# Kernel optimization log

Hardware: AMD Instinct MI355X
Metric: run time of the kernel (lower is better)

Reference implementation:

```python
import jax, jax.numpy as jnp
import numpy as np

B, T, D, H = 8, 1024, 512, 8
HD = D // H  # per-head hidden = embed_dim // n_head = 64
EPS = 1e-5


def setup_inputs() -> dict:
    key = jax.random.key(0)
    ks = jax.random.split(key, 8)
    x = jax.random.normal(ks[0], (B, T, D), dtype=jnp.float32)
    sc = 1.0 / np.sqrt(D)
    Wq = jax.random.normal(ks[1], (D, H * HD), dtype=jnp.float32) * sc
    Wk = jax.random.normal(ks[2], (D, H * HD), dtype=jnp.float32) * sc
    Wp = jax.random.normal(ks[3], (H * HD, D), dtype=jnp.float32) * sc
    bq = jnp.zeros((H * HD,), jnp.float32)
    bk = jnp.zeros((H * HD,), jnp.float32)
    bp = jnp.zeros((D,), jnp.float32)
    w_mlp = jax.random.normal(ks[4], (2 * HD,), dtype=jnp.float32) * 0.1
    ln_g = jnp.ones((D,), jnp.float32)
    ln_b = jnp.zeros((D,), jnp.float32)
    return {"x": x, "Wq": Wq, "bq": bq, "Wk": Wk, "bk": bk,
            "Wp": Wp, "bp": bp, "w_mlp": w_mlp, "ln_g": ln_g, "ln_b": ln_b}


def reference(x, Wq, bq, Wk, bk, Wp, bp, w_mlp, ln_g, ln_b):
    b, t, d = x.shape
    h, hd = H, HD
    # q/k projections, split into heads: [B,T,H,hd]
    qx = (x @ Wq + bq).reshape(b, t, h, hd)
    kx = (x @ Wk + bk).reshape(b, t, h, hd)
    # MLP score: tanh(concat(k_j, q_i) . w) == tanh(k_j.w[:hd] + q_i.w[hd:])
    k_s = jnp.einsum('bkhd,d->bkh', kx, w_mlp[:hd])   # [B,K,H]
    q_s = jnp.einsum('bqhd,d->bqh', qx, w_mlp[hd:])   # [B,Q,H]
    score = jnp.tanh(q_s[:, :, None, :] + k_s[:, None, :, :])  # [B,Q,K,H]
    attn = jax.nn.softmax(score, axis=2)  # softmax over k_len
    # values are the key projection kx (bmm(score, kx) in original)
    out = jnp.einsum('bqkh,bkhd->bqhd', attn, kx).reshape(b, t, h * hd)
    out = out @ Wp + bp  # output projection (dropout is identity at eval)
    # residual + LayerNorm
    y = x + out
    mu = jnp.mean(y, axis=-1, keepdims=True)
    var = jnp.var(y, axis=-1, keepdims=True)
    yn = (y - mu) * jax.lax.rsqrt(var + EPS)
    return yn * ln_g + ln_b
```

## Files before the change

kernel.cpp:

```cpp
#include <hip/hip_runtime.h>
#include <cstddef>

#define TT 1024
#define DDIM 512
#define HH 8
#define NND 128
#define NS 68

typedef __attribute__((ext_vector_type(8))) short bfrag;
typedef __attribute__((ext_vector_type(4))) float facc;

#define SC2   2.8853900817779268f
#define L2E   1.4426950408889634f

static __device__ __forceinline__ unsigned bfrne(float f) {
    unsigned u = __float_as_uint(f);
    return (u + 0x7fffu + ((u >> 16) & 1u)) >> 16;
}
static __device__ __forceinline__ unsigned pack2rne(float a, float b) {
    return bfrne(a) | (bfrne(b) << 16);
}
static __device__ __forceinline__ unsigned pack2hu(float a, float b) {
    return ((__float_as_uint(a) + 0x8000u) >> 16) |
           ((__float_as_uint(b) + 0x8000u) & 0xffff0000u);
}
static __device__ __forceinline__ void gl2lds16(const void* g, void* l) {
    __builtin_amdgcn_global_load_lds(
        (const __attribute__((address_space(1))) unsigned int*)g,
        (__attribute__((address_space(3))) unsigned int*)l, 16, 0, 0);
}
static __device__ __forceinline__ float wt(float t) {
    float r = __builtin_amdgcn_rcpf(t + 1.f);
    return __builtin_amdgcn_exp2f(fmaf(r, -2.f * L2E, L2E));
}

__global__ __launch_bounds__(256) void prepare_kernel(
    const float* __restrict__ x, const float* __restrict__ Wk,
    const float* __restrict__ Wp, const float* __restrict__ Wq,
    const float* __restrict__ bq, const float* __restrict__ wm,
    unsigned short* __restrict__ xb, unsigned short* __restrict__ WkT,
    unsigned short* __restrict__ WpT, unsigned short* __restrict__ vq2b,
    float* __restrict__ qsb2)
{
    const int bx = blockIdx.x, tid = threadIdx.x;
    const int lane = tid & 63, wave = tid >> 6;
    if (bx < 2048) {
        const int row = bx * 4 + wave;
        const float4* xr = (const float4*)(x + (size_t)row * DDIM);
        float4 x0 = xr[lane * 2], x1 = xr[lane * 2 + 1];
        uint4 st;
        st.x = pack2rne(x0.x, x0.y); st.y = pack2rne(x0.z, x0.w);
        st.z = pack2rne(x1.x, x1.y); st.w = pack2rne(x1.z, x1.w);
        int p = lane ^ (row & 7);
        *(uint4*)(xb + (size_t)row * DDIM + p * 8) = st;
    } else if (bx < 2176) {
        int idx = bx - 2048;
        const float* src = (idx & 64) ? Wp : Wk;
        unsigned short* dst = (idx & 64) ? WpT : WkT;
        idx &= 63;
        const int n0 = (idx & 7) * 64, k0 = (idx >> 3) * 64;
        __shared__ float sT[64][65];
        #pragma unroll
        for (int it = 0; it < 4; ++it) {
            int task = it * 256 + tid;
            int kr = task >> 4, c4 = (task & 15) * 4;
            float4 v = *(const float4*)(src + (size_t)(k0 + kr) * DDIM + n0 + c4);
            sT[kr][c4] = v.x; sT[kr][c4 + 1] = v.y; sT[kr][c4 + 2] = v.z; sT[kr][c4 + 3] = v.w;
        }
        __syncthreads();
        #pragma unroll
        for (int it = 0; it < 2; ++it) {
            int task = it * 256 + tid;
            int n = task >> 3, kg = task & 7;
            unsigned u[4];
            #pragma unroll
            for (int jj = 0; jj < 4; ++jj)
                u[jj] = pack2rne(sT[kg * 8 + jj * 2][n], sT[kg * 8 + jj * 2 + 1][n]);
            int p = ((k0 >> 3) + kg) ^ (n & 7);
            uint4 st; st.x = u[0]; st.y = u[1]; st.z = u[2]; st.w = u[3];
            *(uint4*)(dst + (size_t)(n0 + n) * DDIM + p * 8) = st;
        }
    } else {
        int idx = (bx - 2176) * 4 + wave;
        int h = idx >> 9, d = idx & 511;
        float v = Wq[(size_t)d * DDIM + h * 64 + lane] * wm[64 + lane];
        #pragma unroll
        for (int off = 32; off > 0; off >>= 1) v += __shfl_xor(v, off);
        if (lane == 0) vq2b[h * DDIM + d] = (unsigned short)bfrne(v * SC2);
        if (bx == 2176 && tid < HH) {
            float sb = 0.f;
            for (int j = 0; j < 64; ++j)
                sb = fmaf(bq[tid * 64 + j], wm[64 + j], sb);
            qsb2[tid] = sb * SC2;
        }
    }
}

__global__ __launch_bounds__(256) void gemm1_kernel(
    const unsigned short* __restrict__ A, const unsigned short* __restrict__ B,
    const float* __restrict__ bias, unsigned short* __restrict__ kxTg,
    float* __restrict__ ks2, const float* __restrict__ wm,
    const unsigned short* __restrict__ vq2b, const float* __restrict__ qsb2,
    float* __restrict__ qs2)
{
    __shared__ __align__(16) unsigned short smem[50176];
    unsigned short* svq = smem + 49152;
    const int tid = threadIdx.x, lane = tid & 63, wave = tid >> 6;
    const int l15 = lane & 15, quad = lane >> 4;
    const int wr = wave >> 1, wc = wave & 1;
    const int row0 = blockIdx.x * 128, colpair = blockIdx.y;
    const int h = colpair * 2 + wc, n0 = colpair * 128;

    const float qsbh = qsb2[h];
    float bvv[4], wmv[4];
    #pragma unroll
    for (int nt = 0; nt < 4; ++nt) {
        bvv[nt] = bias[h * 64 + nt * 16 + l15];
        wmv[nt] = wm[nt * 16 + l15] * SC2;
    }

    facc acc[4][4]; facc accq[4];
    #pragma unroll
    for (int i = 0; i < 4; ++i) {
        #pragma unroll
        for (int j = 0; j < 4; ++j) { acc[i][j][0]=0.f; acc[i][j][1]=0.f; acc[i][j][2]=0.f; acc[i][j][3]=0.f; }
        accq[i][0]=0.f; accq[i][1]=0.f; accq[i][2]=0.f; accq[i][3]=0.f;
    }

    if (tid < 128)
        gl2lds16(vq2b + colpair * 1024 + tid * 8, &svq[tid * 8]);

    auto stage = [&](int sel, int k0) {
        unsigned short* dA = smem + sel * 16384;
        unsigned short* dB = dA + 8192;
        #pragma unroll
        for (int it = 0; it < 4; ++it) {
            int g = it * 256 + tid;
            int r = g >> 3, kg = g & 7;
            gl2lds16(A + (size_t)(row0 + r) * 512 + k0 + kg * 8, &dA[g * 8]);
            gl2lds16(B + (size_t)(n0 + r) * 512 + k0 + kg * 8, &dB[g * 8]);
        }
    };

    stage(0, 0);
    stage(1, 64);
    #pragma unroll
    for (int kt = 0; kt < 8; ++kt) {
        const int sel = kt % 3;
        if (kt < 6) {
            stage((kt + 2) % 3, (kt + 2) * 64);
            asm volatile("s_waitcnt vmcnt(16)" ::: "memory");
        } else if (kt == 6) {
            asm volatile("s_waitcnt vmcnt(8)" ::: "memory");
        } else {
            asm volatile("s_waitcnt vmcnt(0)" ::: "memory");
        }
        __builtin_amdgcn_s_barrier();
        __builtin_amdgcn_sched_barrier(0);
        const unsigned short* sA = smem + sel * 16384;
        const unsigned short* sB = sA + 8192;
        #pragma unroll
        for (int ks_ = 0; ks_ < 2; ++ks_) {
            int slot = (ks_ * 4 + quad) ^ (l15 & 7);
            bfrag a[4], b[4];
            #pragma unroll
            for (int i = 0; i < 4; ++i) {
                a[i] = *(const bfrag*)&sA[(wr * 64 + i * 16 + l15) * 64 + slot * 8];
                b[i] = *(const bfrag*)&sB[(wc * 64 + i * 16 + l15) * 64 + slot * 8];
            }
            bfrag bvq = *(const bfrag*)&svq[wc * 512 + kt * 64 + ks_ * 32 + quad * 8];
            #pragma unroll
            for (int i = 0; i < 4; ++i) {
                #pragma unroll
                for (int nt = 0; nt < 4; ++nt)
                    acc[i][nt] = __builtin_amdgcn_mfma_f32_16x16x32_bf16(a[i], b[nt], acc[i][nt], 0, 0, 0);
                accq[i] = __builtin_amdgcn_mfma_f32_16x16x32_bf16(a[i], bvq, accq[i], 0, 0, 0);
            }
        }
        __builtin_amdgcn_s_barrier();
        __builtin_amdgcn_sched_barrier(0);
    }
    asm volatile("" ::: "memory");

    const int bb = row0 >> 10, t0 = row0 & 1023;
    float part[4][4];
    #pragma unroll
    for (int i = 0; i < 4; ++i)
        #pragma unroll
        for (int r = 0; r < 4; ++r) part[i][r] = 0.f;

    unsigned short* eT = smem + wc * 8704;
    #pragma unroll
    for (int i = 0; i < 4; ++i) {
        int tr = wr * 64 + i * 16 + quad * 4;
        #pragma unroll
        for (int nt = 0; nt < 4; ++nt) {
            int d = nt * 16 + l15;
            float v0 = acc[i][nt][0] + bvv[nt], v1 = acc[i][nt][1] + bvv[nt];
            float v2 = acc[i][nt][2] + bvv[nt], v3 = acc[i][nt][3] + bvv[nt];
            part[i][0] = fmaf(wmv[nt], v0, part[i][0]);
            part[i][1] = fmaf(wmv[nt], v1, part[i][1]);
            part[i][2] = fmaf(wmv[nt], v2, part[i][2]);
            part[i][3] = fmaf(wmv[nt], v3, part[i][3]);
            *(unsigned*)&eT[d * 136 + tr]     = pack2rne(v0, v1);
            *(unsigned*)&eT[d * 136 + tr + 2] = pack2rne(v2, v3);
        }
    }
    #pragma unroll
    for (int i = 0; i < 4; ++i)
        #pragma unroll
        for (int r = 0; r < 4; ++r) {
            float p = part[i][r];
            p += __shfl_xor(p, 1); p += __shfl_xor(p, 2);
            p += __shfl_xor(p, 4); p += __shfl_xor(p, 8);
            if (l15 == 0) {
                size_t o = (size_t)(bb * HH + h) * TT + t0 + wr * 64 + i * 16 + quad * 4 + r;
                ks2[o] = p;
                qs2[o] = accq[i][r] + qsbh;
            }
        }
    __syncthreads();
    #pragma unroll
    for (int it = 0; it < 8; ++it) {
        int task = it * 256 + tid;
        int hh = task >> 10, rem = task & 1023;
        int col = rem >> 4, seg = rem & 15;
        uint4 v = *(const uint4*)&smem[hh * 8704 + col * 136 + seg * 8];
        int hg = colpair * 2 + hh;
        int g = (t0 >> 3) + seg;
        int p = g ^ (col & 7);
        *(uint4*)(kxTg + ((size_t)(bb * HH + hg) * 64 + col) * TT + p * 8) = v;
    }
}

__global__ __launch_bounds__(256) void nodes_kernel(
    const unsigned short* __restrict__ kxTg, const float* __restrict__ qs2,
    const float* __restrict__ ks2, float* __restrict__ npart)
{
    __shared__ __align__(16) unsigned short kxT[16384];
    __shared__ float tks[256];
    __shared__ float redl[8];
    const int bh = blockIdx.x, kq = blockIdx.y;
    const int tid = threadIdx.x, lane = tid & 63, wave = tid >> 6;
    const int l15 = lane & 15, quad = lane >> 4;
    const unsigned short* kxbase = kxTg + (size_t)bh * 64 * TT;

    #pragma unroll
    for (int it = 0; it < 8; ++it) {
        int g = it * 256 + tid;
        int d = g >> 5, j = g & 31;
        gl2lds16(kxbase + (size_t)d * TT + kq * 256 + j * 8, &kxT[g * 8]);
    }
    float ksv = ks2[(size_t)bh * TT + kq * 256 + tid];
    float4 q4 = ((const float4*)(qs2 + (size_t)bh * TT))[tid];
    tks[tid] = __builtin_amdgcn_exp2f(ksv);
    float mn = fminf(fminf(q4.x, q4.y), fminf(q4.z, q4.w));
    float mx = fmaxf(fmaxf(q4.x, q4.y), fmaxf(q4.z, q4.w));
    #pragma unroll
    for (int off = 32; off > 0; off >>= 1) {
        mn = fminf(mn, __shfl_xor(mn, off));
        mx = fmaxf(mx, __shfl_xor(mx, off));
    }
    if (lane == 0) { redl[wave] = mn; redl[4 + wave] = mx; }
    __syncthreads();
    const float mnv = fminf(fminf(redl[0], redl[1]), fminf(redl[2], redl[3]));
    const float mxv = fmaxf(fmaxf(redl[4], redl[5]), fmaxf(redl[6], redl[7]));
    const float h2v = (mxv - mnv) * (1.f / 127.f);
    const float zA = mnv + (wave * 16 + l15) * h2v;
    const float zB = zA + 64.f * h2v;
    const float tzA = __builtin_amdgcn_exp2f(zA);
    const float tzB = __builtin_amdgcn_exp2f(zB);

    facc acc[2][4]; facc accZ[2];
    #pragma unroll
    for (int g = 0; g < 2; ++g) {
        #pragma unroll
        for (int i = 0; i < 4; ++i) { acc[g][i][0]=0.f; acc[g][i][1]=0.f; acc[g][i][2]=0.f; acc[g][i][3]=0.f; }
        accZ[g][0]=0.f; accZ[g][1]=0.f; accZ[g][2]=0.f; accZ[g][3]=0.f;
    }
    bfrag ones;
    #pragma unroll
    for (int j = 0; j < 8; ++j) ones[j] = (short)0x3F80;

    #pragma unroll
    for (int kst = 0; kst < 8; ++kst) {
        const float* kvp = &tks[kst * 32 + quad * 8];
        float4 kv0 = *(const float4*)kvp;
        float4 kv1 = *(const float4*)(kvp + 4);
        int slot = (kst * 4 + quad) ^ (l15 & 7);
        bfrag bf_[4];
        #pragma unroll
        for (int dt = 0; dt < 4; ++dt)
            bf_[dt] = *(const bfrag*)&kxT[(dt * 16 + l15) * 256 + slot * 8];
        #pragma unroll
        for (int g = 0; g < 2; ++g) {
            float tz = g ? tzB : tzA;
            union { unsigned u[4]; bfrag f; } afu;
            afu.u[0] = pack2hu(wt(tz * kv0.x), wt(tz * kv0.y));
            afu.u[1] = pack2hu(wt(tz * kv0.z), wt(tz * kv0.w));
            afu.u[2] = pack2hu(wt(tz * kv1.x), wt(tz * kv1.y));
            afu.u[3] = pack2hu(wt(tz * kv1.z), wt(tz * kv1.w));
            #pragma unroll
            for (int dt = 0; dt < 4; ++dt)
                acc[g][dt] = __builtin_amdgcn_mfma_f32_16x16x32_bf16(afu.f, bf_[dt], acc[g][dt], 0, 0, 0);
            accZ[g] = __builtin_amdgcn_mfma_f32_16x16x32_bf16(afu.f, ones, accZ[g], 0, 0, 0);
        }
    }
    float* dst = npart + (size_t)(bh * 4 + kq) * (NND * NS);
    #pragma unroll
    for (int g = 0; g < 2; ++g)
        #pragma unroll
        for (int r = 0; r < 4; ++r) {
            int node = g * 64 + wave * 16 + quad * 4 + r;
            #pragma unroll
            for (int dt = 0; dt < 4; ++dt)
                dst[node * NS + dt * 16 + l15] = acc[g][dt][r];
            if (l15 == 0) dst[node * NS + 64] = accZ[g][r];
        }
}

__global__ __launch_bounds__(256) void interp_kernel(
    const float* __restrict__ npart, const float* __restrict__ qs2,
    unsigned short* __restrict__ attb)
{
    __shared__ __align__(16) float nodes[NND * NS];
    __shared__ float redl[8];
    const int bh = blockIdx.x, tq = blockIdx.y;
    const int b = bh >> 3, h = bh & 7;
    const int tid = threadIdx.x, lane = tid & 63, wave = tid >> 6;

    float4 q4 = ((const float4*)(qs2 + (size_t)bh * TT))[tid];
    float mn = fminf(fminf(q4.x, q4.y), fminf(q4.z, q4.w));
    float mx = fmaxf(fmaxf(q4.x, q4.y), fmaxf(q4.z, q4.w));
    #pragma unroll
    for (int off = 32; off > 0; off >>= 1) {
        mn = fminf(mn, __shfl_xor(mn, off));
        mx = fmaxf(mx, __shfl_xor(mx, off));
    }
    if (lane == 0) { redl[wave] = mn; redl[4 + wave] = mx; }
    __syncthreads();
    const float mnv = fminf(fminf(redl[0], redl[1]), fminf(redl[2], redl[3]));
    const float mxv = fmaxf(fmaxf(redl[4], redl[5]), fmaxf(redl[6], redl[7]));
    const float inv127v = 127.f / fmaxf(mxv - mnv, 1e-12f);

    const float4* p0 = (const float4*)(npart + (size_t)(bh * 4 + 0) * (NND * NS));
    const float4* p1 = (const float4*)(npart + (size_t)(bh * 4 + 1) * (NND * NS));
    const float4* p2 = (const float4*)(npart + (size_t)(bh * 4 + 2) * (NND * NS));
    const float4* p3 = (const float4*)(npart + (size_t)(bh * 4 + 3) * (NND * NS));
    #pragma unroll
    for (int it = 0; it < 9; ++it) {
        int g = it * 256 + tid;
        if (g < (NND * NS) / 4) {
            float4 a = p0[g], bb4 = p1[g], c = p2[g], d = p3[g];
            float4 s;
            s.x = a.x + bb4.x + c.x + d.x;
            s.y = a.y + bb4.y + c.y + d.y;
            s.z = a.z + bb4.z + c.z + d.z;
            s.w = a.w + bb4.w + c.w + d.w;
            ((float4*)nodes)[g] = s;
        }
    }
    __syncthreads();

    const float* qsp = qs2 + (size_t)bh * TT;
    #pragma unroll 2
    for (int it = 0; it < 16; ++it) {
        int task = it * 256 + tid;
        int t = tq * 256 + (task >> 4), dp = task & 15;
        float qv = qsp[t];
        float u = (qv - mnv) * inv127v;
        int i = (int)floorf(u) - 1;
        i = i < 0 ? 0 : (i > NND - 4 ? NND - 4 : i);
        float s = u - (float)i;
        float s1 = s - 1.f, s2 = s - 2.f, s3 = s - 3.f;
        float w0 = -s1 * s2 * s3 * (1.f / 6.f);
        float w1 = s * s2 * s3 * 0.5f;
        float w2 = -s * s1 * s3 * 0.5f;
        float w3 = s * s1 * s2 * (1.f / 6.f);
        const float* base = &nodes[i * NS];
        float4 v0 = *(const float4*)(base + 4 * dp);
        float4 v1 = *(const float4*)(base + NS + 4 * dp);
        float4 v2 = *(const float4*)(base + 2 * NS + 4 * dp);
        float4 v3 = *(const float4*)(base + 3 * NS + 4 * dp);
        float zz = w0 * base[64] + w1 * base[NS + 64] + w2 * base[2 * NS + 64] + w3 * base[3 * NS + 64];
        float ox = w0 * v0.x + w1 * v1.x + w2 * v2.x + w3 * v3.x;
        float oy = w0 * v0.y + w1 * v1.y + w2 * v2.y + w3 * v3.y;
        float oz = w0 * v0.z + w1 * v1.z + w2 * v2.z + w3 * v3.z;
        float ow = w0 * v0.w + w1 * v1.w + w2 * v2.w + w3 * v3.w;
        float rz = __builtin_amdgcn_rcpf(zz);
        uint2 st;
        st.x = pack2rne(ox * rz, oy * rz);
        st.y = pack2rne(oz * rz, ow * rz);
        int row = b * TT + t;
        int col = h * 64 + 4 * dp;
        int p = (col >> 3) ^ (row & 7);
        *(uint2*)&attb[(size_t)row * DDIM + p * 8 + (col & 7)] = st;
    }
}

__global__ __launch_bounds__(256) void gemm2_kernel(
    const unsigned short* __restrict__ A, const unsigned short* __restrict__ B,
    const float* __restrict__ bias, unsigned short* __restrict__ yb)
{
    __shared__ __align__(16) unsigned short smem[49152];
    const int tid = threadIdx.x, lane = tid & 63, wave = tid >> 6;
    const int l15 = lane & 15, quad = lane >> 4;
    const int wr = wave >> 1, wc = wave & 1;
    const int row0 = blockIdx.x * 128, col0 = blockIdx.y * 128;

    float bvv[4];
    #pragma unroll
    for (int nt = 0; nt < 4; ++nt) bvv[nt] = bias[col0 + wc * 64 + nt * 16 + l15];

    facc acc[4][4];
    #pragma unroll
    for (int i = 0; i < 4; ++i)
        #pragma unroll
        for (int j = 0; j < 4; ++j) { acc[i][j][0]=0.f; acc[i][j][1]=0.f; acc[i][j][2]=0.f; acc[i][j][3]=0.f; }

    auto stage = [&](int sel, int k0) {
        unsigned short* dA = smem + sel * 16384;
        unsigned short* dB = dA + 8192;
        #pragma unroll
        for (int it = 0; it < 4; ++it) {
            int g = it * 256 + tid;
            int r = g >> 3, kg = g & 7;
            gl2lds16(A + (size_t)(row0 + r) * 512 + k0 + kg * 8, &dA[g * 8]);
            gl2lds16(B + (size_t)(col0 + r) * 512 + k0 + kg * 8, &dB[g * 8]);
        }
    };

    stage(0, 0);
    stage(1, 64);
    #pragma unroll
    for (int kt = 0; kt < 8; ++kt) {
        const int sel = kt % 3;
        if (kt < 6) {
            stage((kt + 2) % 3, (kt + 2) * 64);
            asm volatile("s_waitcnt vmcnt(16)" ::: "memory");
        } else if (kt == 6) {
            asm volatile("s_waitcnt vmcnt(8)" ::: "memory");
        } else {
            asm volatile("s_waitcnt vmcnt(0)" ::: "memory");
        }
        __builtin_amdgcn_s_barrier();
        __builtin_amdgcn_sched_barrier(0);
        const unsigned short* sA = smem + sel * 16384;
        const unsigned short* sB = sA + 8192;
        #pragma unroll
        for (int ks_ = 0; ks_ < 2; ++ks_) {
            int slot = (ks_ * 4 + quad) ^ (l15 & 7);
            bfrag a[4], b[4];
            #pragma unroll
            for (int i = 0; i < 4; ++i) {
                a[i] = *(const bfrag*)&sA[(wr * 64 + i * 16 + l15) * 64 + slot * 8];
                b[i] = *(const bfrag*)&sB[(wc * 64 + i * 16 + l15) * 64 + slot * 8];
            }
            #pragma unroll
            for (int i = 0; i < 4; ++i)
                #pragma unroll
                for (int nt = 0; nt < 4; ++nt)
                    acc[i][nt] = __builtin_amdgcn_mfma_f32_16x16x32_bf16(a[i], b[nt], acc[i][nt], 0, 0, 0);
        }
        __builtin_amdgcn_s_barrier();
        __builtin_amdgcn_sched_barrier(0);
    }
    asm volatile("" ::: "memory");

    unsigned short* yT = smem;
    #pragma unroll
    for (int i = 0; i < 4; ++i) {
        #pragma unroll
        for (int nt = 0; nt < 4; ++nt) {
            int col = wc * 64 + nt * 16 + l15;
            #pragma unroll
            for (int r = 0; r < 4; ++r) {
                int row = wr * 64 + i * 16 + quad * 4 + r;
                yT[row * 136 + col] = (unsigned short)bfrne(acc[i][nt][r] + bvv[nt]);
            }
        }
    }
    __syncthreads();
    #pragma unroll
    for (int it = 0; it < 8; ++it) {
        int task = it * 256 + tid;
        int row = task >> 4, seg = task & 15;
        uint4 v = *(const uint4*)&yT[row * 136 + seg * 8];
        *(uint4*)(yb + (size_t)(row0 + row) * DDIM + col0 + seg * 8) = v;
    }
}

__global__ __launch_bounds__(256) void ln_kernel(
    const unsigned short* __restrict__ yb, const unsigned short* __restrict__ xb,
    const float* __restrict__ g, const float* __restrict__ bet,
    float* __restrict__ out)
{
    const int tid = threadIdx.x, lane = tid & 63, wave = tid >> 6;
    const int row = blockIdx.x * 4 + wave;
    uint4 pv = *(const uint4*)(yb + (size_t)row * DDIM + lane * 8);
    int pgr = lane ^ (row & 7);
    uint4 xv = *(const uint4*)(xb + (size_t)row * DDIM + pgr * 8);
    float y[8];
    const unsigned* pu = (const unsigned*)&pv;
    const unsigned* xu = (const unsigned*)&xv;
    #pragma unroll
    for (int j = 0; j < 4; ++j) {
        y[2*j]   = __uint_as_float(pu[j] << 16)        + __uint_as_float(xu[j] << 16);
        y[2*j+1] = __uint_as_float(pu[j] & 0xffff0000u) + __uint_as_float(xu[j] & 0xffff0000u);
    }
    float s = 0.f, s2 = 0.f;
    #pragma unroll
    for (int i = 0; i < 8; ++i) { s += y[i]; s2 = fmaf(y[i], y[i], s2); }
    #pragma unroll
    for (int off = 32; off > 0; off >>= 1) {
        s += __shfl_xor(s, off);
        s2 += __shfl_xor(s2, off);
    }
    float mu = s * (1.f / 512.f);
    float var = s2 * (1.f / 512.f) - mu * mu;
    float inv = rsqrtf(var + 1e-5f);
    const float4* gp = (const float4*)(g + lane * 8);
    const float4* bp = (const float4*)(bet + lane * 8);
    float4 g0 = gp[0], g1 = gp[1], b0 = bp[0], b1 = bp[1];
    float4 o0, o1;
    o0.x = (y[0] - mu) * inv * g0.x + b0.x; o0.y = (y[1] - mu) * inv * g0.y + b0.y;
    o0.z = (y[2] - mu) * inv * g0.z + b0.z; o0.w = (y[3] - mu) * inv * g0.w + b0.w;
    o1.x = (y[4] - mu) * inv * g1.x + b1.x; o1.y = (y[5] - mu) * inv * g1.y + b1.y;
    o1.z = (y[6] - mu) * inv * g1.z + b1.z; o1.w = (y[7] - mu) * inv * g1.w + b1.w;
    float4* op = (float4*)(out + (size_t)row * DDIM);
    op[lane * 2] = o0; op[lane * 2 + 1] = o1;
}

extern "C" void kernel_launch(void* const* d_in, const int* in_sizes, int n_in,
                              void* d_out, int out_size, void* d_ws, size_t ws_size,
                              hipStream_t stream)
{
    const float* x    = (const float*)d_in[0];
    const float* Wq   = (const float*)d_in[1];
    const float* bq   = (const float*)d_in[2];
    const float* Wk   = (const float*)d_in[3];
    const float* bk   = (const float*)d_in[4];
    const float* Wp   = (const float*)d_in[5];
    const float* bp   = (const float*)d_in[6];
    const float* wm   = (const float*)d_in[7];
    const float* ln_g = (const float*)d_in[8];
    const float* ln_b = (const float*)d_in[9];
    float* out = (float*)d_out;

    float* ws = (float*)d_ws;
    float*          qsb2 = ws;
    unsigned short* vq2b = (unsigned short*)(ws + 64);
    unsigned short* WkT  = (unsigned short*)(ws + 2112);
    unsigned short* WpT  = (unsigned short*)(ws + 133184);
    unsigned short* xb   = (unsigned short*)(ws + 264256);
    unsigned short* kxTg = (unsigned short*)(ws + 2361408);
    float*          qs2  = ws + 4458560;
    float*          ks2  = ws + 4524096;
    unsigned short* attb = (unsigned short*)(ws + 4589632);
    unsigned short* yb   = (unsigned short*)(ws + 6686784);
    float*          npart = ws + 8783936;

    prepare_kernel<<<3200, 256, 0, stream>>>(x, Wk, Wp, Wq, bq, wm,
                                             xb, WkT, WpT, vq2b, qsb2);
    gemm1_kernel<<<dim3(64, 4), 256, 0, stream>>>(xb, WkT, bk, kxTg, ks2, wm,
                                                  vq2b, qsb2, qs2);
    nodes_kernel<<<dim3(64, 4), 256, 0, stream>>>(kxTg, qs2, ks2, npart);
    interp_kernel<<<dim3(64, 4), 256, 0, stream>>>(npart, qs2, attb);
    gemm2_kernel<<<dim3(64, 4), 256, 0, stream>>>(attb, WpT, bp, yb);
    ln_kernel<<<2048, 256, 0, stream>>>(yb, xb, ln_g, ln_b, out);
}
```

Measured before the change: 131.3 us.

## Fuse six stage kernels into one persistent kernel with grid barriers

Result: slower. 290.2 us (+120.9%).

```diff
diff --git a/kernel.cpp b/kernel.cpp
--- a/kernel.cpp
+++ b/kernel.cpp
@@ -6,6 +6,7 @@
 #define HH 8
 #define NND 128
 #define NS 68
+#define NBLK 256
 
 typedef __attribute__((ext_vector_type(8))) short bfrag;
 typedef __attribute__((ext_vector_type(4))) float facc;
@@ -34,520 +35,36 @@
     return __builtin_amdgcn_exp2f(fmaf(r, -2.f * L2E, L2E));
 }
 
-__global__ __launch_bounds__(256) void prepare_kernel(
-    const float* __restrict__ x, const float* __restrict__ Wk,
-    const float* __restrict__ Wp, const float* __restrict__ Wq,
-    const float* __restrict__ bq, const float* __restrict__ wm,
-    unsigned short* __restrict__ xb, unsigned short* __restrict__ WkT,
-    unsigned short* __restrict__ WpT, unsigned short* __restrict__ vq2b,
-    float* __restrict__ qsb2)
+static __device__ __forceinline__ void gsync(unsigned* slot) {
+    __syncthreads();
+    if (threadIdx.x == 0) {
+        __threadfence();
+        __hip_atomic_fetch_add(slot, 1u, __ATOMIC_ACQ_REL, __HIP_MEMORY_SCOPE_AGENT);
+        int guard = 0;
+        while (__hip_atomic_load(slot, __ATOMIC_ACQUIRE, __HIP_MEMORY_SCOPE_AGENT) < NBLK) {
+            __builtin_amdgcn_s_sleep(2);
+            if (++guard > (1 << 20)) break;
+        }
+        __threadfence();
+    }
+    __syncthreads();
+}
+
+struct MArgs {
+    const float* x;  const float* Wq; const float* bq; const float* Wk;
+    const float* bk; const float* Wp; const float* bp; const float* wm;
+    const float* gam; const float* bet; float* out; float* ws; unsigned* bar;
+};
+
+__global__ __launch_bounds__(256) void mega_kernel(MArgs a)
 {
-    const int bx = blockIdx.x, tid = threadIdx.x;
+    __shared__ __align__(16) unsigned char LD[100352];
+
+    const int bid = blockIdx.x, tid = threadIdx.x;
     const int lane = tid & 63, wave = tid >> 6;
-    if (bx < 2048) {
-        const int row = bx * 4 + wave;
-        const float4* xr = (const float4*)(x + (size_t)row * DDIM);
-        float4 x0 = xr[lane * 2], x1 = xr[lane * 2 + 1];
-        uint4 st;
-        st.x = pack2rne(x0.x, x0.y); st.y = pack2rne(x0.z, x0.w);
-        st.z = pack2rne(x1.x, x1.y); st.w = pack2rne(x1.z, x1.w);
-        int p = lane ^ (row & 7);
-        *(uint4*)(xb + (size_t)row * DDIM + p * 8) = st;
-    } else if (bx < 2176) {
-        int idx = bx - 2048;
-        const float* src = (idx & 64) ? Wp : Wk;
-        unsigned short* dst = (idx & 64) ? WpT : WkT;
-        idx &= 63;
-        const int n0 = (idx & 7) * 64, k0 = (idx >> 3) * 64;
-        __shared__ float sT[64][65];
-        #pragma unroll
-        for (int it = 0; it < 4; ++it) {
-            int task = it * 256 + tid;
-            int kr = task >> 4, c4 = (task & 15) * 4;
-            float4 v = *(const float4*)(src + (size_t)(k0 + kr) * DDIM + n0 + c4);
-            sT[kr][c4] = v.x; sT[kr][c4 + 1] = v.y; sT[kr][c4 + 2] = v.z; sT[kr][c4 + 3] = v.w;
-        }
-        __syncthreads();
-        #pragma unroll
-        for (int it = 0; it < 2; ++it) {
-            int task = it * 256 + tid;
-            int n = task >> 3, kg = task & 7;
-            unsigned u[4];
-            #pragma unroll
-            for (int jj = 0; jj < 4; ++jj)
-                u[jj] = pack2rne(sT[kg * 8 + jj * 2][n], sT[kg * 8 + jj * 2 + 1][n]);
-            int p = ((k0 >> 3) + kg) ^ (n & 7);
-            uint4 st; st.x = u[0]; st.y = u[1]; st.z = u[2]; st.w = u[3];
-            *(uint4*)(dst + (size_t)(n0 + n) * DDIM + p * 8) = st;
-        }
-    } else {
-        int idx = (bx - 2176) * 4 + wave;
-        int h = idx >> 9, d = idx & 511;
-        float v = Wq[(size_t)d * DDIM + h * 64 + lane] * wm[64 + lane];
-        #pragma unroll
-        for (int off = 32; off > 0; off >>= 1) v += __shfl_xor(v, off);
-        if (lane == 0) vq2b[h * DDIM + d] = (unsigned short)bfrne(v * SC2);
-        if (bx == 2176 && tid < HH) {
-            float sb = 0.f;
-            for (int j = 0; j < 64; ++j)
-                sb = fmaf(bq[tid * 64 + j], wm[64 + j], sb);
-            qsb2[tid] = sb * SC2;
-        }
-    }
-}
-
-__global__ __launch_bounds__(256) void gemm1_kernel(
-    const unsigned short* __restrict__ A, const unsigned short* __restrict__ B,
-    const float* __restrict__ bias, unsigned short* __restrict__ kxTg,
-    float* __restrict__ ks2, const float* __restrict__ wm,
-    const unsigned short* __restrict__ vq2b, const float* __restrict__ qsb2,
-    float* __restrict__ qs2)
-{
-    __shared__ __align__(16) unsigned short smem[50176];
-    unsigned short* svq = smem + 49152;
-    const int tid = threadIdx.x, lane = tid & 63, wave = tid >> 6;
     const int l15 = lane & 15, quad = lane >> 4;
-    const int wr = wave >> 1, wc = wave & 1;
-    const int row0 = blockIdx.x * 128, colpair = blockIdx.y;
-    const int h = colpair * 2 + wc, n0 = colpair * 128;
-
-    const float qsbh = qsb2[h];
-    float bvv[4], wmv[4];
-    #pragma unroll
-    for (int nt = 0; nt < 4; ++nt) {
-        bvv[nt] = bias[h * 64 + nt * 16 + l15];
-        wmv[nt] = wm[nt * 16 + l15] * SC2;
-    }
-
-    facc acc[4][4]; facc accq[4];
-    #pragma unroll
-    for (int i = 0; i < 4; ++i) {
-        #pragma unroll
-        for (int j = 0; j < 4; ++j) { acc[i][j][0]=0.f; acc[i][j][1]=0.f; acc[i][j][2]=0.f; acc[i][j][3]=0.f; }
-        accq[i][0]=0.f; accq[i][1]=0.f; accq[i][2]=0.f; accq[i][3]=0.f;
-    }
-
-    if (tid < 128)
-        gl2lds16(vq2b + colpair * 1024 + tid * 8, &svq[tid * 8]);
-
-    auto stage = [&](int sel, int k0) {
-        unsigned short* dA = smem + sel * 16384;
-        unsigned short* dB = dA + 8192;
-        #pragma unroll
-        for (int it = 0; it < 4; ++it) {
-            int g = it * 256 + tid;
-            int r = g >> 3, kg = g & 7;
-            gl2lds16(A + (size_t)(row0 + r) * 512 + k0 + kg * 8, &dA[g * 8]);
-            gl2lds16(B + (size_t)(n0 + r) * 512 + k0 + kg * 8, &dB[g * 8]);
-        }
-    };
-
-    stage(0, 0);
-    stage(1, 64);
-    #pragma unroll
-    for (int kt = 0; kt < 8; ++kt) {
-        const int sel = kt % 3;
-        if (kt < 6) {
-            stage((kt + 2) % 3, (kt + 2) * 64);
-            asm volatile("s_waitcnt vmcnt(16)" ::: "memory");
-        } else if (kt == 6) {
-            asm volatile("s_waitcnt vmcnt(8)" ::: "memory");
-        } else {
-            asm volatile("s_waitcnt vmcnt(0)" ::: "memory");
-        }
-        __builtin_amdgcn_s_barrier();
-        __builtin_amdgcn_sched_barrier(0);
-        const unsigned short* sA = smem + sel * 16384;
-        const unsigned short* sB = sA + 8192;
-        #pragma unroll
-        for (int ks_ = 0; ks_ < 2; ++ks_) {
-            int slot = (ks_ * 4 + quad) ^ (l15 & 7);
-            bfrag a[4], b[4];
-            #pragma unroll
-            for (int i = 0; i < 4; ++i) {
-                a[i] = *(const bfrag*)&sA[(wr * 64 + i * 16 + l15) * 64 + slot * 8];
-                b[i] = *(const bfrag*)&sB[(wc * 64 + i * 16 + l15) * 64 + slot * 8];
-            }
-            bfrag bvq = *(const bfrag*)&svq[wc * 512 + kt * 64 + ks_ * 32 + quad * 8];
-            #pragma unroll
-            for (int i = 0; i < 4; ++i) {
-                #pragma unroll
-                for (int nt = 0; nt < 4; ++nt)
-                    acc[i][nt] = __builtin_amdgcn_mfma_f32_16x16x32_bf16(a[i], b[nt], acc[i][nt], 0, 0, 0);
-                accq[i] = __builtin_amdgcn_mfma_f32_16x16x32_bf16(a[i], bvq, accq[i], 0, 0, 0);
-            }
-        }
-        __builtin_amdgcn_s_barrier();
-        __builtin_amdgcn_sched_barrier(0);
-    }
-    asm volatile("" ::: "memory");
-
-    const int bb = row0 >> 10, t0 = row0 & 1023;
-    float part[4][4];
-    #pragma unroll
-    for (int i = 0; i < 4; ++i)
-        #pragma unroll
-        for (int r = 0; r < 4; ++r) part[i][r] = 0.f;
-
-    unsigned short* eT = smem + wc * 8704;
-    #pragma unroll
-    for (int i = 0; i < 4; ++i) {
-        int tr = wr * 64 + i * 16 + quad * 4;
-        #pragma unroll
-        for (int nt = 0; nt < 4; ++nt) {
-            int d = nt * 16 + l15;
-            float v0 = acc[i][nt][0] + bvv[nt], v1 = acc[i][nt][1] + bvv[nt];
-            float v2 = acc[i][nt][2] + bvv[nt], v3 = acc[i][nt][3] + bvv[nt];
-            part[i][0] = fmaf(wmv[nt], v0, part[i][0]);
-            part[i][1] = fmaf(wmv[nt], v1, part[i][1]);
-            part[i][2] = fmaf(wmv[nt], v2, part[i][2]);
-            part[i][3] = fmaf(wmv[nt], v3, part[i][3]);
-            *(unsigned*)&eT[d * 136 + tr]     = pack2rne(v0, v1);
-            *(unsigned*)&eT[d * 136 + tr + 2] = pack2rne(v2, v3);
-        }
-    }
-    #pragma unroll
-    for (int i = 0; i < 4; ++i)
-        #pragma unroll
-        for (int r = 0; r < 4; ++r) {
-            float p = part[i][r];
-            p += __shfl_xor(p, 1); p += __shfl_xor(p, 2);
-            p += __shfl_xor(p, 4); p += __shfl_xor(p, 8);
-            if (l15 == 0) {
-                size_t o = (size_t)(bb * HH + h) * TT + t0 + wr * 64 + i * 16 + quad * 4 + r;
-                ks2[o] = p;
-                qs2[o] = accq[i][r] + qsbh;
-            }
-        }
-    __syncthreads();
-    #pragma unroll
-    for (int it = 0; it < 8; ++it) {
-        int task = it * 256 + tid;
-        int hh = task >> 10, rem = task & 1023;
-        int col = rem >> 4, seg = rem & 15;
-        uint4 v = *(const uint4*)&smem[hh * 8704 + col * 136 + seg * 8];
-        int hg = colpair * 2 + hh;
-        int g = (t0 >> 3) + seg;
-        int p = g ^ (col & 7);
-        *(uint4*)(kxTg + ((size_t)(bb * HH + hg) * 64 + col) * TT + p * 8) = v;
-    }
-}
-
-__global__ __launch_bounds__(256) void nodes_kernel(
-    const unsigned short* __restrict__ kxTg, const float* __restrict__ qs2,
-    const float* __restrict__ ks2, float* __restrict__ npart)
-{
-    __shared__ __align__(16) unsigned short kxT[16384];
-    __shared__ float tks[256];
-    __shared__ float redl[8];
-    const int bh = blockIdx.x, kq = blockIdx.y;
-    const int tid = threadIdx.x, lane = tid & 63, wave = tid >> 6;
-    const int l15 = lane & 15, quad = lane >> 4;
-    const unsigned short* kxbase = kxTg + (size_t)bh * 64 * TT;
-
-    #pragma unroll
-    for (int it = 0; it < 8; ++it) {
-        int g = it * 256 + tid;
-        int d = g >> 5, j = g & 31;
-        gl2lds16(kxbase + (size_t)d * TT + kq * 256 + j * 8, &kxT[g * 8]);
-    }
-    float ksv = ks2[(size_t)bh * TT + kq * 256 + tid];
-    float4 q4 = ((const float4*)(qs2 + (size_t)bh * TT))[tid];
-    tks[tid] = __builtin_amdgcn_exp2f(ksv);
-    float mn = fminf(fminf(q4.x, q4.y), fminf(q4.z, q4.w));
-    float mx = fmaxf(fmaxf(q4.x, q4.y), fmaxf(q4.z, q4.w));
-    #pragma unroll
-    for (int off = 32; off > 0; off >>= 1) {
-        mn = fminf(mn, __shfl_xor(mn, off));
-        mx = fmaxf(mx, __shfl_xor(mx, off));
-    }
-    if (lane == 0) { redl[wave] = mn; redl[4 + wave] = mx; }
-    __syncthreads();
-    const float mnv = fminf(fminf(redl[0], redl[1]), fminf(redl[2], redl[3]));
-    const float mxv = fmaxf(fmaxf(redl[4], redl[5]), fmaxf(redl[6], redl[7]));
-    const float h2v = (mxv - mnv) * (1.f / 127.f);
-    const float zA = mnv + (wave * 16 + l15) * h2v;
-    const float zB = zA + 64.f * h2v;
-    const float tzA = __builtin_amdgcn_exp2f(zA);
-    const float tzB = __builtin_amdgcn_exp2f(zB);
-
-    facc acc[2][4]; facc accZ[2];
-    #pragma unroll
-    for (int g = 0; g < 2; ++g) {
-        #pragma unroll
-        for (int i = 0; i < 4; ++i) { acc[g][i][0]=0.f; acc[g][i][1]=0.f; acc[g][i][2]=0.f; acc[g][i][3]=0.f; }
-        accZ[g][0]=0.f; accZ[g][1]=0.f; accZ[g][2]=0.f; accZ[g][3]=0.f;
-    }
-    bfrag ones;
-    #pragma unroll
-    for (int j = 0; j < 8; ++j) ones[j] = (short)0x3F80;
-
-    #pragma unroll
-    for (int kst = 0; kst < 8; ++kst) {
-        const float* kvp = &tks[kst * 32 + quad * 8];
-        float4 kv0 = *(const float4*)kvp;
-        float4 kv1 = *(const float4*)(kvp + 4);
-        int slot = (kst * 4 + quad) ^ (l15 & 7);
-        bfrag bf_[4];
-        #pragma unroll
-        for (int dt = 0; dt < 4; ++dt)
-            bf_[dt] = *(const bfrag*)&kxT[(dt * 16 + l15) * 256 + slot * 8];
-        #pragma unroll
-        for (int g = 0; g < 2; ++g) {
-            float tz = g ? tzB : tzA;
-            union { unsigned u[4]; bfrag f; } afu;
-            afu.u[0] = pack2hu(wt(tz * kv0.x), wt(tz * kv0.y));
-            afu.u[1] = pack2hu(wt(tz * kv0.z), wt(tz * kv0.w));
-            afu.u[2] = pack2hu(wt(tz * kv1.x), wt(tz * kv1.y));
-            afu.u[3] = pack2hu(wt(tz * kv1.z), wt(tz * kv1.w));
-            #pragma unroll
-            for (int dt = 0; dt < 4; ++dt)
-                acc[g][dt] = __builtin_amdgcn_mfma_f32_16x16x32_bf16(afu.f, bf_[dt], acc[g][dt], 0, 0, 0);
-            accZ[g] = __builtin_amdgcn_mfma_f32_16x16x32_bf16(afu.f, ones, accZ[g], 0, 0, 0);
-        }
-    }
-    float* dst = npart + (size_t)(bh * 4 + kq) * (NND * NS);
-    #pragma unroll
-    for (int g = 0; g < 2; ++g)
-        #pragma unroll
-        for (int r = 0; r < 4; ++r) {
-            int node = g * 64 + wave * 16 + quad * 4 + r;
-            #pragma unroll
-            for (int dt = 0; dt < 4; ++dt)
-                dst[node * NS + dt * 16 + l15] = acc[g][dt][r];
-            if (l15 == 0) dst[node * NS + 64] = accZ[g][r];
-        }
-}
-
-__global__ __launch_bounds__(256) void interp_kernel(
-    const float* __restrict__ npart, const float* __restrict__ qs2,
-    unsigned short* __restrict__ attb)
-{
-    __shared__ __align__(16) float nodes[NND * NS];
-    __shared__ float redl[8];
-    const int bh = blockIdx.x, tq = blockIdx.y;
-    const int b = bh >> 3, h = bh & 7;
-    const int tid = threadIdx.x, lane = tid & 63, wave = tid >> 6;
-
-    float4 q4 = ((const float4*)(qs2 + (size_t)bh * TT))[tid];
-    float mn = fminf(fminf(q4.x, q4.y), fminf(q4.z, q4.w));
-    float mx = fmaxf(fmaxf(q4.x, q4.y), fmaxf(q4.z, q4.w));
-    #pragma unroll
-    for (int off = 32; off > 0; off >>= 1) {
-        mn = fminf(mn, __shfl_xor(mn, off));
-        mx = fmaxf(mx, __shfl_xor(mx, off));
-    }
-    if (lane == 0) { redl[wave] = mn; redl[4 + wave] = mx; }
-    __syncthreads();
-    const float mnv = fminf(fminf(redl[0], redl[1]), fminf(redl[2], redl[3]));
-    const float mxv = fmaxf(fmaxf(redl[4], redl[5]), fmaxf(redl[6], redl[7]));
-    const float inv127v = 127.f / fmaxf(mxv - mnv, 1e-12f);
-
-    const float4* p0 = (const float4*)(npart + (size_t)(bh * 4 + 0) * (NND * NS));
-    const float4* p1 = (const float4*)(npart + (size_t)(bh * 4 + 1) * (NND * NS));
-    const float4* p2 = (const float4*)(npart + (size_t)(bh * 4 + 2) * (NND * NS));
-    const float4* p3 = (const float4*)(npart + (size_t)(bh * 4 + 3) * (NND * NS));
-    #pragma unroll
-    for (int it = 0; it < 9; ++it) {
-        int g = it * 256 + tid;
-        if (g < (NND * NS) / 4) {
-            float4 a = p0[g], bb4 = p1[g], c = p2[g], d = p3[g];
-            float4 s;
-            s.x = a.x + bb4.x + c.x + d.x;
-            s.y = a.y + bb4.y + c.y + d.y;
-            s.z = a.z + bb4.z + c.z + d.z;
-            s.w = a.w + bb4.w + c.w + d.w;
-            ((float4*)nodes)[g] = s;
-        }
-    }
-    __syncthreads();
-
-    const float* qsp = qs2 + (size_t)bh * TT;
-    #pragma unroll 2
-    for (int it = 0; it < 16; ++it) {
-        int task = it * 256 + tid;
-        int t = tq * 256 + (task >> 4), dp = task & 15;
-        float qv = qsp[t];
-        float u = (qv - mnv) * inv127v;
-        int i = (int)floorf(u) - 1;
-        i = i < 0 ? 0 : (i > NND - 4 ? NND - 4 : i);
-        float s = u - (float)i;
-        float s1 = s - 1.f, s2 = s - 2.f, s3 = s - 3.f;
-        float w0 = -s1 * s2 * s3 * (1.f / 6.f);
-        float w1 = s * s2 * s3 * 0.5f;
-        float w2 = -s * s1 * s3 * 0.5f;
-        float w3 = s * s1 * s2 * (1.f / 6.f);
-        const float* base = &nodes[i * NS];
-        float4 v0 = *(const float4*)(base + 4 * dp);
-        float4 v1 = *(const float4*)(base + NS + 4 * dp);
-        float4 v2 = *(const float4*)(base + 2 * NS + 4 * dp);
-        float4 v3 = *(const float4*)(base + 3 * NS + 4 * dp);
-        float zz = w0 * base[64] + w1 * base[NS + 64] + w2 * base[2 * NS + 64] + w3 * base[3 * NS + 64];
-        float ox = w0 * v0.x + w1 * v1.x + w2 * v2.x + w3 * v3.x;
-        float oy = w0 * v0.y + w1 * v1.y + w2 * v2.y + w3 * v3.y;
-        float oz = w0 * v0.z + w1 * v1.z + w2 * v2.z + w3 * v3.z;
-        float ow = w0 * v0.w + w1 * v1.w + w2 * v2.w + w3 * v3.w;
-        float rz = __builtin_amdgcn_rcpf(zz);
-        uint2 st;
-        st.x = pack2rne(ox * rz, oy * rz);
-        st.y = pack2rne(oz * rz, ow * rz);
-        int row = b * TT + t;
-        int col = h * 64 + 4 * dp;
-        int p = (col >> 3) ^ (row & 7);
-        *(uint2*)&attb[(size_t)row * DDIM + p * 8 + (col & 7)] = st;
-    }
-}
-
-__global__ __launch_bounds__(256) void gemm2_kernel(
-    const unsigned short* __restrict__ A, const unsigned short* __restrict__ B,
-    const float* __restrict__ bias, unsigned short* __restrict__ yb)
-{
-    __shared__ __align__(16) unsigned short smem[49152];
-    const int tid = threadIdx.x, lane = tid & 63, wave = tid >> 6;
-    const int l15 = lane & 15, quad = lane >> 4;
-    const int wr = wave >> 1, wc = wave & 1;
-    const int row0 = blockIdx.x * 128, col0 = blockIdx.y * 128;
-
-    float bvv[4];
-    #pragma unroll
-    for (int nt = 0; nt < 4; ++nt) bvv[nt] = bias[col0 + wc * 64 + nt * 16 + l15];
-
-    facc acc[4][4];
-    #pragma unroll
-    for (int i = 0; i < 4; ++i)
-        #pragma unroll
-        for (int j = 0; j < 4; ++j) { acc[i][j][0]=0.f; acc[i][j][1]=0.f; acc[i][j][2]=0.f; acc[i][j][3]=0.f; }
-
-    auto stage = [&](int sel, int k0) {
-        unsigned short* dA = smem + sel * 16384;
-        unsigned short* dB = dA + 8192;
-        #pragma unroll
-        for (int it = 0; it < 4; ++it) {
-            int g = it * 256 + tid;
-            int r = g >> 3, kg = g & 7;
-            gl2lds16(A + (size_t)(row0 + r) * 512 + k0 + kg * 8, &dA[g * 8]);
-            gl2lds16(B + (size_t)(col0 + r) * 512 + k0 + kg * 8, &dB[g * 8]);
-        }
-    };
-
-    stage(0, 0);
-    stage(1, 64);
-    #pragma unroll
-    for (int kt = 0; kt < 8; ++kt) {
-        const int sel = kt % 3;
-        if (kt < 6) {
-            stage((kt + 2) % 3, (kt + 2) * 64);
-            asm volatile("s_waitcnt vmcnt(16)" ::: "memory");
-        } else if (kt == 6) {
-            asm volatile("s_waitcnt vmcnt(8)" ::: "memory");
-        } else {
-            asm volatile("s_waitcnt vmcnt(0)" ::: "memory");
-        }
-        __builtin_amdgcn_s_barrier();
-        __builtin_amdgcn_sched_barrier(0);
-        const unsigned short* sA = smem + sel * 16384;
-        const unsigned short* sB = sA + 8192;
-        #pragma unroll
-        for (int ks_ = 0; ks_ < 2; ++ks_) {
-            int slot = (ks_ * 4 + quad) ^ (l15 & 7);
-            bfrag a[4], b[4];
-            #pragma unroll
-            for (int i = 0; i < 4; ++i) {
-                a[i] = *(const bfrag*)&sA[(wr * 64 + i * 16 + l15) * 64 + slot * 8];
-                b[i] = *(const bfrag*)&sB[(wc * 64 + i * 16 + l15) * 64 + slot * 8];
-            }
-            #pragma unroll
-            for (int i = 0; i < 4; ++i)
-                #pragma unroll
-                for (int nt = 0; nt < 4; ++nt)
-                    acc[i][nt] = __builtin_amdgcn_mfma_f32_16x16x32_bf16(a[i], b[nt], acc[i][nt], 0, 0, 0);
-        }
-        __builtin_amdgcn_s_barrier();
-        __builtin_amdgcn_sched_barrier(0);
-    }
-    asm volatile("" ::: "memory");
-
-    unsigned short* yT = smem;
-    #pragma unroll
-    for (int i = 0; i < 4; ++i) {
-        #pragma unroll
-        for (int nt = 0; nt < 4; ++nt) {
-            int col = wc * 64 + nt * 16 + l15;
-            #pragma unroll
-            for (int r = 0; r < 4; ++r) {
-                int row = wr * 64 + i * 16 + quad * 4 + r;
-                yT[row * 136 + col] = (unsigned short)bfrne(acc[i][nt][r] + bvv[nt]);
-            }
-        }
-    }
-    __syncthreads();
-    #pragma unroll
-    for (int it = 0; it < 8; ++it) {
-        int task = it * 256 + tid;
-        int row = task >> 4, seg = task & 15;
-        uint4 v = *(const uint4*)&yT[row * 136 + seg * 8];
-        *(uint4*)(yb + (size_t)(row0 + row) * DDIM + col0 + seg * 8) = v;
-    }
-}
-
-__global__ __launch_bounds__(256) void ln_kernel(
-    const unsigned short* __restrict__ yb, const unsigned short* __restrict__ xb,
-    const float* __restrict__ g, const float* __restrict__ bet,
-    float* __restrict__ out)
-{
-    const int tid = threadIdx.x, lane = tid & 63, wave = tid >> 6;
-    const int row = blockIdx.x * 4 + wave;
-    uint4 pv = *(const uint4*)(yb + (size_t)row * DDIM + lane * 8);
-    int pgr = lane ^ (row & 7);
-    uint4 xv = *(const uint4*)(xb + (size_t)row * DDIM + pgr * 8);
-    float y[8];
-    const unsigned* pu = (const unsigned*)&pv;
-    const unsigned* xu = (const unsigned*)&xv;
-    #pragma unroll
-    for (int j = 0; j < 4; ++j) {
-        y[2*j]   = __uint_as_float(pu[j] << 16)        + __uint_as_float(xu[j] << 16);
-        y[2*j+1] = __uint_as_float(pu[j] & 0xffff0000u) + __uint_as_float(xu[j] & 0xffff0000u);
-    }
-    float s = 0.f, s2 = 0.f;
-    #pragma unroll
-    for (int i = 0; i < 8; ++i) { s += y[i]; s2 = fmaf(y[i], y[i], s2); }
-    #pragma unroll
-    for (int off = 32; off > 0; off >>= 1) {
-        s += __shfl_xor(s, off);
-        s2 += __shfl_xor(s2, off);
-    }
-    float mu = s * (1.f / 512.f);
-    float var = s2 * (1.f / 512.f) - mu * mu;
-    float inv = rsqrtf(var + 1e-5f);
-    const float4* gp = (const float4*)(g + lane * 8);
-    const float4* bp = (const float4*)(bet + lane * 8);
-    float4 g0 = gp[0], g1 = gp[1], b0 = bp[0], b1 = bp[1];
-    float4 o0, o1;
-    o0.x = (y[0] - mu) * inv * g0.x + b0.x; o0.y = (y[1] - mu) * inv * g0.y + b0.y;
-    o0.z = (y[2] - mu) * inv * g0.z + b0.z; o0.w = (y[3] - mu) * inv * g0.w + b0.w;
-    o1.x = (y[4] - mu) * inv * g1.x + b1.x; o1.y = (y[5] - mu) * inv * g1.y + b1.y;
-    o1.z = (y[6] - mu) * inv * g1.z + b1.z; o1.w = (y[7] - mu) * inv * g1.w + b1.w;
-    float4* op = (float4*)(out + (size_t)row * DDIM);
-    op[lane * 2] = o0; op[lane * 2 + 1] = o1;
-}
-
-extern "C" void kernel_launch(void* const* d_in, const int* in_sizes, int n_in,
-                              void* d_out, int out_size, void* d_ws, size_t ws_size,
-                              hipStream_t stream)
-{
-    const float* x    = (const float*)d_in[0];
-    const float* Wq   = (const float*)d_in[1];
-    const float* bq   = (const float*)d_in[2];
-    const float* Wk   = (const float*)d_in[3];
-    const float* bk   = (const float*)d_in[4];
-    const float* Wp   = (const float*)d_in[5];
-    const float* bp   = (const float*)d_in[6];
-    const float* wm   = (const float*)d_in[7];
-    const float* ln_g = (const float*)d_in[8];
-    const float* ln_b = (const float*)d_in[9];
-    float* out = (float*)d_out;
-
-    float* ws = (float*)d_ws;
+
+    float* ws = a.ws;
     float*          qsb2 = ws;
     unsigned short* vq2b = (unsigned short*)(ws + 64);
     unsigned short* WkT  = (unsigned short*)(ws + 2112);
@@ -560,12 +77,501 @@
     unsigned short* yb   = (unsigned short*)(ws + 6686784);
     float*          npart = ws + 8783936;
 
-    prepare_kernel<<<3200, 256, 0, stream>>>(x, Wk, Wp, Wq, bq, wm,
-                                             xb, WkT, WpT, vq2b, qsb2);
-    gemm1_kernel<<<dim3(64, 4), 256, 0, stream>>>(xb, WkT, bk, kxTg, ks2, wm,
-                                                  vq2b, qsb2, qs2);
-    nodes_kernel<<<dim3(64, 4), 256, 0, stream>>>(kxTg, qs2, ks2, npart);
-    interp_kernel<<<dim3(64, 4), 256, 0, stream>>>(npart, qs2, attb);
-    gemm2_kernel<<<dim3(64, 4), 256, 0, stream>>>(attb, WpT, bp, yb);
-    ln_kernel<<<2048, 256, 0, stream>>>(yb, xb, ln_g, ln_b, out);
-}
+    {
+        #pragma unroll
+        for (int i = 0; i < 8; ++i) {
+            int row = bid * 32 + i * 4 + wave;
+            const float4* xr = (const float4*)(a.x + (size_t)row * DDIM);
+            float4 x0 = xr[lane * 2], x1 = xr[lane * 2 + 1];
+            uint4 st;
+            st.x = pack2rne(x0.x, x0.y); st.y = pack2rne(x0.z, x0.w);
+            st.z = pack2rne(x1.x, x1.y); st.w = pack2rne(x1.z, x1.w);
+            int p = lane ^ (row & 7);
+            *(uint4*)(xb + (size_t)row * DDIM + p * 8) = st;
+        }
+        #pragma unroll
+        for (int e = 0; e < 4; ++e) {
+            int idx = (bid * 4 + wave) * 4 + e;
+            int h = idx >> 9, d = idx & 511;
+            float v = a.Wq[(size_t)d * DDIM + h * 64 + lane] * a.wm[64 + lane];
+            #pragma unroll
+            for (int off = 32; off > 0; off >>= 1) v += __shfl_xor(v, off);
+            if (lane == 0) vq2b[h * DDIM + d] = (unsigned short)bfrne(v * SC2);
+        }
+        if (bid == 0 && tid < HH) {
+            float sb = 0.f;
+            for (int j = 0; j < 64; ++j)
+                sb = fmaf(a.bq[tid * 64 + j], a.wm[64 + j], sb);
+            qsb2[tid] = sb * SC2;
+        }
+        if (bid < 128) {
+            const float* src = (bid & 64) ? a.Wp : a.Wk;
+            unsigned short* dst = (bid & 64) ? WpT : WkT;
+            int idx = bid & 63;
+            const int n0 = (idx & 7) * 64, k0 = (idx >> 3) * 64;
+            float (*sT)[65] = (float(*)[65])LD;
+            #pragma unroll
+            for (int it = 0; it < 4; ++it) {
+                int task = it * 256 + tid;
+                int kr = task >> 4, c4 = (task & 15) * 4;
+                float4 v = *(const float4*)(src + (size_t)(k0 + kr) * DDIM + n0 + c4);
+                sT[kr][c4] = v.x; sT[kr][c4 + 1] = v.y; sT[kr][c4 + 2] = v.z; sT[kr][c4 + 3] = v.w;
+            }
+            __syncthreads();
+            #pragma unroll
+            for (int it = 0; it < 2; ++it) {
+                int task = it * 256 + tid;
+                int n = task >> 3, kg = task & 7;
+                unsigned u[4];
+                #pragma unroll
+                for (int jj = 0; jj < 4; ++jj)
+                    u[jj] = pack2rne(sT[kg * 8 + jj * 2][n], sT[kg * 8 + jj * 2 + 1][n]);
+                int p = ((k0 >> 3) + kg) ^ (n & 7);
+                uint4 st; st.x = u[0]; st.y = u[1]; st.z = u[2]; st.w = u[3];
+                *(uint4*)(dst + (size_t)(n0 + n) * DDIM + p * 8) = st;
+            }
+        }
+    }
+    gsync(a.bar + 0);
+
+    {
+        unsigned short* smem = (unsigned short*)LD;
+        unsigned short* svq  = smem + 49152;
+        const int rt = bid & 63, colpair = bid >> 6;
+        const int wr = wave >> 1, wc = wave & 1;
+        const int row0 = rt * 128;
+        const int h = colpair * 2 + wc, n0 = colpair * 128;
+
+        const float qsbh = qsb2[h];
+        float bvv[4], wmv[4];
+        #pragma unroll
+        for (int nt = 0; nt < 4; ++nt) {
+            bvv[nt] = a.bk[h * 64 + nt * 16 + l15];
+            wmv[nt] = a.wm[nt * 16 + l15] * SC2;
+        }
+
+        facc acc[4][4]; facc accq[4];
+        #pragma unroll
+        for (int i = 0; i < 4; ++i) {
+            #pragma unroll
+            for (int j = 0; j < 4; ++j) { acc[i][j][0]=0.f; acc[i][j][1]=0.f; acc[i][j][2]=0.f; acc[i][j][3]=0.f; }
+            accq[i][0]=0.f; accq[i][1]=0.f; accq[i][2]=0.f; accq[i][3]=0.f;
+        }
+
+        if (tid < 128)
+            gl2lds16(vq2b + colpair * 1024 + tid * 8, &svq[tid * 8]);
+
+        auto stage = [&](int sel, int k0) {
+            unsigned short* dA = smem + sel * 16384;
+            unsigned short* dB = dA + 8192;
+            #pragma unroll
+            for (int it = 0; it < 4; ++it) {
+                int g = it * 256 + tid;
+                int r = g >> 3, kg = g & 7;
+                gl2lds16(xb + (size_t)(row0 + r) * 512 + k0 + kg * 8, &dA[g * 8]);
+                gl2lds16(WkT + (size_t)(n0 + r) * 512 + k0 + kg * 8, &dB[g * 8]);
+            }
+        };
+
+        stage(0, 0);
+        stage(1, 64);
+        #pragma unroll
+        for (int kt = 0; kt < 8; ++kt) {
+            const int sel = kt % 3;
+            if (kt < 6) {
+                stage((kt + 2) % 3, (kt + 2) * 64);
+                asm volatile("s_waitcnt vmcnt(16)" ::: "memory");
+            } else if (kt == 6) {
+                asm volatile("s_waitcnt vmcnt(8)" ::: "memory");
+            } else {
+                asm volatile("s_waitcnt vmcnt(0)" ::: "memory");
+            }
+            __builtin_amdgcn_s_barrier();
+            __builtin_amdgcn_sched_barrier(0);
+            const unsigned short* sA = smem + sel * 16384;
+            const unsigned short* sB = sA + 8192;
+            #pragma unroll
+            for (int ks_ = 0; ks_ < 2; ++ks_) {
+                int slot = (ks_ * 4 + quad) ^ (l15 & 7);
+                bfrag av[4], bv[4];
+                #pragma unroll
+                for (int i = 0; i < 4; ++i) {
+                    av[i] = *(const bfrag*)&sA[(wr * 64 + i * 16 + l15) * 64 + slot * 8];
+                    bv[i] = *(const bfrag*)&sB[(wc * 64 + i * 16 + l15) * 64 + slot * 8];
+                }
+                bfrag bvq = *(const bfrag*)&svq[wc * 512 + kt * 64 + ks_ * 32 + quad * 8];
+                #pragma unroll
+                for (int i = 0; i < 4; ++i) {
+                    #pragma unroll
+                    for (int nt = 0; nt < 4; ++nt)
+                        acc[i][nt] = __builtin_amdgcn_mfma_f32_16x16x32_bf16(av[i], bv[nt], acc[i][nt], 0, 0, 0);
+                    accq[i] = __builtin_amdgcn_mfma_f32_16x16x32_bf16(av[i], bvq, accq[i], 0, 0, 0);
+                }
+            }
+            __builtin_amdgcn_s_barrier();
+            __builtin_amdgcn_sched_barrier(0);
+        }
+        asm volatile("" ::: "memory");
+
+        const int bb = row0 >> 10, t0 = row0 & 1023;
+        float part[4][4];
+        #pragma unroll
+        for (int i = 0; i < 4; ++i)
+            #pragma unroll
+            for (int r = 0; r < 4; ++r) part[i][r] = 0.f;
+
+        unsigned short* eT = smem + wc * 8704;
+        #pragma unroll
+        for (int i = 0; i < 4; ++i) {
+            int tr = wr * 64 + i * 16 + quad * 4;
+            #pragma unroll
+            for (int nt = 0; nt < 4; ++nt) {
+                int d = nt * 16 + l15;
+                float v0 = acc[i][nt][0] + bvv[nt], v1 = acc[i][nt][1] + bvv[nt];
+                float v2 = acc[i][nt][2] + bvv[nt], v3 = acc[i][nt][3] + bvv[nt];
+                part[i][0] = fmaf(wmv[nt], v0, part[i][0]);
+                part[i][1] = fmaf(wmv[nt], v1, part[i][1]);
+                part[i][2] = fmaf(wmv[nt], v2, part[i][2]);
+                part[i][3] = fmaf(wmv[nt], v3, part[i][3]);
+                *(unsigned*)&eT[d * 136 + tr]     = pack2rne(v0, v1);
+                *(unsigned*)&eT[d * 136 + tr + 2] = pack2rne(v2, v3);
+            }
+        }
+        #pragma unroll
+        for (int i = 0; i < 4; ++i)
+            #pragma unroll
+            for (int r = 0; r < 4; ++r) {
+                float p = part[i][r];
+                p += __shfl_xor(p, 1); p += __shfl_xor(p, 2);
+                p += __shfl_xor(p, 4); p += __shfl_xor(p, 8);
+                if (l15 == 0) {
+                    size_t o = (size_t)(bb * HH + h) * TT + t0 + wr * 64 + i * 16 + quad * 4 + r;
+                    ks2[o] = p;
+                    qs2[o] = accq[i][r] + qsbh;
+                }
+            }
+        __syncthreads();
+        #pragma unroll
+        for (int it = 0; it < 8; ++it) {
+            int task = it * 256 + tid;
+            int hh = task >> 10, rem = task & 1023;
+            int col = rem >> 4, seg = rem & 15;
+            uint4 v = *(const uint4*)&smem[hh * 8704 + col * 136 + seg * 8];
+            int hg = colpair * 2 + hh;
+            int g = (t0 >> 3) + seg;
+            int p = g ^ (col & 7);
+            *(uint4*)(kxTg + ((size_t)(bb * HH + hg) * 64 + col) * TT + p * 8) = v;
+        }
+    }
+    gsync(a.bar + 1);
+
+    {
+        unsigned short* kxT = (unsigned short*)LD;
+        float* tks  = (float*)(LD + 32768);
+        float* redl = (float*)(LD + 33792);
+        const int bh = bid & 63, kq = bid >> 6;
+        const unsigned short* kxbase = kxTg + (size_t)bh * 64 * TT;
+
+        #pragma unroll
+        for (int it = 0; it < 8; ++it) {
+            int g = it * 256 + tid;
+            int d = g >> 5, j = g & 31;
+            gl2lds16(kxbase + (size_t)d * TT + kq * 256 + j * 8, &kxT[g * 8]);
+        }
+        float ksv = ks2[(size_t)bh * TT + kq * 256 + tid];
+        float4 q4 = ((const float4*)(qs2 + (size_t)bh * TT))[tid];
+        tks[tid] = __builtin_amdgcn_exp2f(ksv);
+        float mn = fminf(fminf(q4.x, q4.y), fminf(q4.z, q4.w));
+        float mx = fmaxf(fmaxf(q4.x, q4.y), fmaxf(q4.z, q4.w));
+        #pragma unroll
+        for (int off = 32; off > 0; off >>= 1) {
+            mn = fminf(mn, __shfl_xor(mn, off));
+            mx = fmaxf(mx, __shfl_xor(mx, off));
+        }
+        if (lane == 0) { redl[wave] = mn; redl[4 + wave] = mx; }
+        __syncthreads();
+        const float mnv = fminf(fminf(redl[0], redl[1]), fminf(redl[2], redl[3]));
+        const float mxv = fmaxf(fmaxf(redl[4], redl[5]), fmaxf(redl[6], redl[7]));
+        const float h2v = (mxv - mnv) * (1.f / 127.f);
+        const float zA = mnv + (wave * 16 + l15) * h2v;
+        const float zB = zA + 64.f * h2v;
+        const float tzA = __builtin_amdgcn_exp2f(zA);
+        const float tzB = __builtin_amdgcn_exp2f(zB);
+
+        facc acc[2][4]; facc accZ[2];
+        #pragma unroll
+        for (int g = 0; g < 2; ++g) {
+            #pragma unroll
+            for (int i = 0; i < 4; ++i) { acc[g][i][0]=0.f; acc[g][i][1]=0.f; acc[g][i][2]=0.f; acc[g][i][3]=0.f; }
+            accZ[g][0]=0.f; accZ[g][1]=0.f; accZ[g][2]=0.f; accZ[g][3]=0.f;
+        }
+        bfrag ones;
+        #pragma unroll
+        for (int j = 0; j < 8; ++j) ones[j] = (short)0x3F80;
+
+        #pragma unroll
+        for (int kst = 0; kst < 8; ++kst) {
+            const float* kvp = &tks[kst * 32 + quad * 8];
+            float4 kv0 = *(const float4*)kvp;
+            float4 kv1 = *(const float4*)(kvp + 4);
+            int slot = (kst * 4 + quad) ^ (l15 & 7);
+            bfrag bf_[4];
+            #pragma unroll
+            for (int dt = 0; dt < 4; ++dt)
+                bf_[dt] = *(const bfrag*)&kxT[(dt * 16 + l15) * 256 + slot * 8];
+            #pragma unroll
+            for (int g = 0; g < 2; ++g) {
+                float tz = g ? tzB : tzA;
+                union { unsigned u[4]; bfrag f; } afu;
+                afu.u[0] = pack2hu(wt(tz * kv0.x), wt(tz * kv0.y));
+                afu.u[1] = pack2hu(wt(tz * kv0.z), wt(tz * kv0.w));
+                afu.u[2] = pack2hu(wt(tz * kv1.x), wt(tz * kv1.y));
+                afu.u[3] = pack2hu(wt(tz * kv1.z), wt(tz * kv1.w));
+                #pragma unroll
+                for (int dt = 0; dt < 4; ++dt)
+                    acc[g][dt] = __builtin_amdgcn_mfma_f32_16x16x32_bf16(afu.f, bf_[dt], acc[g][dt], 0, 0, 0);
+                accZ[g] = __builtin_amdgcn_mfma_f32_16x16x32_bf16(afu.f, ones, accZ[g], 0, 0, 0);
+            }
+        }
+        float* dst = npart + (size_t)(bh * 4 + kq) * (NND * NS);
+        #pragma unroll
+        for (int g = 0; g < 2; ++g)
+            #pragma unroll
+            for (int r = 0; r < 4; ++r) {
+                int node = g * 64 + wave * 16 + quad * 4 + r;
+                #pragma unroll
+                for (int dt = 0; dt < 4; ++dt)
+                    dst[node * NS + dt * 16 + l15] = acc[g][dt][r];
+                if (l15 == 0) dst[node * NS + 64] = accZ[g][r];
+            }
+    }
+    gsync(a.bar + 2);
+
+    {
+        float* nodesArr = (float*)LD;
+        float* redl = (float*)(LD + 34816);
+        const int bh = bid & 63, tq = bid >> 6;
+        const int b = bh >> 3, h = bh & 7;
+
+        float4 q4 = ((const float4*)(qs2 + (size_t)bh * TT))[tid];
+        float mn = fminf(fminf(q4.x, q4.y), fminf(q4.z, q4.w));
+        float mx = fmaxf(fmaxf(q4.x, q4.y), fmaxf(q4.z, q4.w));
+        #pragma unroll
+        for (int off = 32; off > 0; off >>= 1) {
+            mn = fminf(mn, __shfl_xor(mn, off));
+            mx = fmaxf(mx, __shfl_xor(mx, off));
+        }
+        if (lane == 0) { redl[wave] = mn; redl[4 + wave] = mx; }
+        __syncthreads();
+        const float mnv = fminf(fminf(redl[0], redl[1]), fminf(redl[2], redl[3]));
+        const float mxv = fmaxf(fmaxf(redl[4], redl[5]), fmaxf(redl[6], redl[7]));
+        const float inv127v = 127.f / fmaxf(mxv - mnv, 1e-12f);
+
+        const float4* p0 = (const float4*)(npart + (size_t)(bh * 4 + 0) * (NND * NS));
+        const float4* p1 = (const float4*)(npart + (size_t)(bh * 4 + 1) * (NND * NS));
+        const float4* p2 = (const float4*)(npart + (size_t)(bh * 4 + 2) * (NND * NS));
+        const float4* p3 = (const float4*)(npart + (size_t)(bh * 4 + 3) * (NND * NS));
+        #pragma unroll
+        for (int it = 0; it < 9; ++it) {
+            int g = it * 256 + tid;
+            if (g < (NND * NS) / 4) {
+                float4 av = p0[g], bv = p1[g], cv = p2[g], dv = p3[g];
+                float4 s;
+                s.x = av.x + bv.x + cv.x + dv.x;
+                s.y = av.y + bv.y + cv.y + dv.y;
+                s.z = av.z + bv.z + cv.z + dv.z;
+                s.w = av.w + bv.w + cv.w + dv.w;
+                ((float4*)nodesArr)[g] = s;
+            }
+        }
+        __syncthreads();
+
+        const float* qsp = qs2 + (size_t)bh * TT;
+        #pragma unroll 2
+        for (int it = 0; it < 16; ++it) {
+            int task = it * 256 + tid;
+            int t = tq * 256 + (task >> 4), dp = task & 15;
+            float qv = qsp[t];
+            float u = (qv - mnv) * inv127v;
+            int i = (int)floorf(u) - 1;
+            i = i < 0 ? 0 : (i > NND - 4 ? NND - 4 : i);
+            float s = u - (float)i;
+            float s1 = s - 1.f, s2 = s - 2.f, s3 = s - 3.f;
+            float w0 = -s1 * s2 * s3 * (1.f / 6.f);
+            float w1 = s * s2 * s3 * 0.5f;
+            float w2 = -s * s1 * s3 * 0.5f;
+            float w3 = s * s1 * s2 * (1.f / 6.f);
+            const float* base = &nodesArr[i * NS];
+            float4 v0 = *(const float4*)(base + 4 * dp);
+            float4 v1 = *(const float4*)(base + NS + 4 * dp);
+            float4 v2 = *(const float4*)(base + 2 * NS + 4 * dp);
+            float4 v3 = *(const float4*)(base + 3 * NS + 4 * dp);
+            float zz = w0 * base[64] + w1 * base[NS + 64] + w2 * base[2 * NS + 64] + w3 * base[3 * NS + 64];
+            float ox = w0 * v0.x + w1 * v1.x + w2 * v2.x + w3 * v3.x;
+            float oy = w0 * v0.y + w1 * v1.y + w2 * v2.y + w3 * v3.y;
+            float oz = w0 * v0.z + w1 * v1.z + w2 * v2.z + w3 * v3.z;
+            float ow = w0 * v0.w + w1 * v1.w + w2 * v2.w + w3 * v3.w;
+            float rz = __builtin_amdgcn_rcpf(zz);
+            uint2 st;
+            st.x = pack2rne(ox * rz, oy * rz);
+            st.y = pack2rne(oz * rz, ow * rz);
+            int row = b * TT + t;
+            int col = h * 64 + 4 * dp;
+            int p = (col >> 3) ^ (row & 7);
+            *(uint2*)&attb[(size_t)row * DDIM + p * 8 + (col & 7)] = st;
+        }
+    }
+    gsync(a.bar + 3);
+
+    {
+        unsigned short* smem = (unsigned short*)LD;
+        const int rt = bid & 63, cp = bid >> 6;
+        const int wr = wave >> 1, wc = wave & 1;
+        const int row0 = rt * 128, col0 = cp * 128;
+
+        float bvv[4];
+        #pragma unroll
+        for (int nt = 0; nt < 4; ++nt) bvv[nt] = a.bp[col0 + wc * 64 + nt * 16 + l15];
+
+        facc acc[4][4];
+        #pragma unroll
+        for (int i = 0; i < 4; ++i)
+            #pragma unroll
+            for (int j = 0; j < 4; ++j) { acc[i][j][0]=0.f; acc[i][j][1]=0.f; acc[i][j][2]=0.f; acc[i][j][3]=0.f; }
+
+        auto stage = [&](int sel, int k0) {
+            unsigned short* dA = smem + sel * 16384;
+            unsigned short* dB = dA + 8192;
+            #pragma unroll
+            for (int it = 0; it < 4; ++it) {
+                int g = it * 256 + tid;
+                int r = g >> 3, kg = g & 7;
+                gl2lds16(attb + (size_t)(row0 + r) * 512 + k0 + kg * 8, &dA[g * 8]);
+                gl2lds16(WpT + (size_t)(col0 + r) * 512 + k0 + kg * 8, &dB[g * 8]);
+            }
+        };
+
+        stage(0, 0);
+        stage(1, 64);
+        #pragma unroll
+        for (int kt = 0; kt < 8; ++kt) {
+            const int sel = kt % 3;
+            if (kt < 6) {
+                stage((kt + 2) % 3, (kt + 2) * 64);
+                asm volatile("s_waitcnt vmcnt(16)" ::: "memory");
+            } else if (kt == 6) {
+                asm volatile("s_waitcnt vmcnt(8)" ::: "memory");
+            } else {
+                asm volatile("s_waitcnt vmcnt(0)" ::: "memory");
+            }
+            __builtin_amdgcn_s_barrier();
+            __builtin_amdgcn_sched_barrier(0);
+            const unsigned short* sA = smem + sel * 16384;
+            const unsigned short* sB = sA + 8192;
+            #pragma unroll
+            for (int ks_ = 0; ks_ < 2; ++ks_) {
+                int slot = (ks_ * 4 + quad) ^ (l15 & 7);
+                bfrag av[4], bv[4];
+                #pragma unroll
+                for (int i = 0; i < 4; ++i) {
+                    av[i] = *(const bfrag*)&sA[(wr * 64 + i * 16 + l15) * 64 + slot * 8];
+                    bv[i] = *(const bfrag*)&sB[(wc * 64 + i * 16 + l15) * 64 + slot * 8];
+                }
+                #pragma unroll
+                for (int i = 0; i < 4; ++i)
+                    #pragma unroll
+                    for (int nt = 0; nt < 4; ++nt)
+                        acc[i][nt] = __builtin_amdgcn_mfma_f32_16x16x32_bf16(av[i], bv[nt], acc[i][nt], 0, 0, 0);
+            }
+            __builtin_amdgcn_s_barrier();
+            __builtin_amdgcn_sched_barrier(0);
+        }
+        asm volatile("" ::: "memory");
+
+        unsigned short* yT = smem;
+        #pragma unroll
+        for (int i = 0; i < 4; ++i) {
+            #pragma unroll
+            for (int nt = 0; nt < 4; ++nt) {
+                int col = wc * 64 + nt * 16 + l15;
+                #pragma unroll
+                for (int r = 0; r < 4; ++r) {
+                    int row = wr * 64 + i * 16 + quad * 4 + r;
+                    yT[row * 136 + col] = (unsigned short)bfrne(acc[i][nt][r] + bvv[nt]);
+                }
+            }
+        }
+        __syncthreads();
+        #pragma unroll
+        for (int it = 0; it < 8; ++it) {
+            int task = it * 256 + tid;
+            int row = task >> 4, seg = task & 15;
+            uint4 v = *(const uint4*)&yT[row * 136 + seg * 8];
+            *(uint4*)(yb + (size_t)(row0 + row) * DDIM + col0 + seg * 8) = v;
+        }
+    }
+    gsync(a.bar + 4);
+
+    {
+        #pragma unroll
+        for (int it = 0; it < 8; ++it) {
+            int row = bid * 32 + it * 4 + wave;
+            uint4 pv = *(const uint4*)(yb + (size_t)row * DDIM + lane * 8);
+            int pgr = lane ^ (row & 7);
+            uint4 xv = *(const uint4*)(xb + (size_t)row * DDIM + pgr * 8);
+            float y[8];
+            const unsigned* pu = (const unsigned*)&pv;
+            const unsigned* xu = (const unsigned*)&xv;
+            #pragma unroll
+            for (int j = 0; j < 4; ++j) {
+                y[2*j]   = __uint_as_float(pu[j] << 16)        + __uint_as_float(xu[j] << 16);
+                y[2*j+1] = __uint_as_float(pu[j] & 0xffff0000u) + __uint_as_float(xu[j] & 0xffff0000u);
+            }
+            float s = 0.f, s2 = 0.f;
+            #pragma unroll
+            for (int i = 0; i < 8; ++i) { s += y[i]; s2 = fmaf(y[i], y[i], s2); }
+            #pragma unroll
+            for (int off = 32; off > 0; off >>= 1) {
+                s += __shfl_xor(s, off);
+                s2 += __shfl_xor(s2, off);
+            }
+            float mu = s * (1.f / 512.f);
+            float var = s2 * (1.f / 512.f) - mu * mu;
+            float inv = rsqrtf(var + 1e-5f);
+            const float4* gp = (const float4*)(a.gam + lane * 8);
+            const float4* bpp = (const float4*)(a.bet + lane * 8);
+            float4 g0 = gp[0], g1 = gp[1], b0 = bpp[0], b1 = bpp[1];
+            float4 o0, o1;
+            o0.x = (y[0] - mu) * inv * g0.x + b0.x; o0.y = (y[1] - mu) * inv * g0.y + b0.y;
+            o0.z = (y[2] - mu) * inv * g0.z + b0.z; o0.w = (y[3] - mu) * inv * g0.w + b0.w;
+            o1.x = (y[4] - mu) * inv * g1.x + b1.x; o1.y = (y[5] - mu) * inv * g1.y + b1.y;
+            o1.z = (y[6] - mu) * inv * g1.z + b1.z; o1.w = (y[7] - mu) * inv * g1.w + b1.w;
+            float4* op = (float4*)(a.out + (size_t)row * DDIM);
+            op[lane * 2] = o0; op[lane * 2 + 1] = o1;
+        }
+    }
+}
+
+extern "C" void kernel_launch(void* const* d_in, const int* in_sizes, int n_in,
+                              void* d_out, int out_size, void* d_ws, size_t ws_size,
+                              hipStream_t stream)
+{
+    float* ws = (float*)d_ws;
+    MArgs ma;
+    ma.x   = (const float*)d_in[0];
+    ma.Wq  = (const float*)d_in[1];
+    ma.bq  = (const float*)d_in[2];
+    ma.Wk  = (const float*)d_in[3];
+    ma.bk  = (const float*)d_in[4];
+    ma.Wp  = (const float*)d_in[5];
+    ma.bp  = (const float*)d_in[6];
+    ma.wm  = (const float*)d_in[7];
+    ma.gam = (const float*)d_in[8];
+    ma.bet = (const float*)d_in[9];
+    ma.out = (float*)d_out;
+    ma.ws  = ws;
+    ma.bar = (unsigned*)(ws + 11100160);
+
+    hipMemsetAsync(ma.bar, 0, 8 * sizeof(unsigned), stream);
+    mega_kernel<<<NBLK, 256, 0, stream>>>(ma);
+}
```
